# Optimization experiments

Measured on AMD Instinct MI355X. Metric: run time of the kernel, lower is better.

## Reference

```python
import jax, jax.numpy as jnp
import numpy as np

# canonical SMPL kinematic tree (24 joints)
PARENTS = [-1, 0, 0, 0, 1, 2, 3, 4, 5, 6, 7, 8, 9, 9, 9, 12, 13, 14, 16, 17, 18, 19, 20, 21]
B, V, J, NB = 512, 6890, 24, 10


def setup_inputs() -> dict:
    key = jax.random.key(0)
    ks = jax.random.split(key, 9)
    betas = jax.random.normal(ks[0], (B, NB), jnp.float32)
    body_pose = 0.3 * jax.random.normal(ks[1], (B, (J - 1) * 3), jnp.float32)
    global_orient = 0.3 * jax.random.normal(ks[2], (B, 3), jnp.float32)
    transl = jax.random.normal(ks[3], (B, 3), jnp.float32)
    v_template = jax.random.normal(ks[4], (V, 3), jnp.float32)
    shapedirs = 0.01 * jax.random.normal(ks[5], (V, 3, NB), jnp.float32)
    posedirs = 0.01 * jax.random.normal(ks[6], (9 * (J - 1), V * 3), jnp.float32)
    J_regressor = jax.nn.softmax(4.0 * jax.random.normal(ks[7], (J, V), jnp.float32), axis=-1)
    lbs_weights = jax.nn.softmax(4.0 * jax.random.normal(ks[8], (V, J), jnp.float32), axis=-1)
    return {"betas": betas, "body_pose": body_pose, "global_orient": global_orient,
            "transl": transl, "v_template": v_template, "shapedirs": shapedirs,
            "posedirs": posedirs, "J_regressor": J_regressor, "lbs_weights": lbs_weights}


def rodrigues(rot_vecs):
    # rot_vecs: [B, J, 3] axis-angle -> [B, J, 3, 3] rotation matrices
    angle = jnp.linalg.norm(rot_vecs + 1e-8, axis=-1, keepdims=True)  # [B,J,1]
    axis = rot_vecs / angle
    s = jnp.sin(angle)[..., None]
    c = jnp.cos(angle)[..., None]
    x, y, z = axis[..., 0], axis[..., 1], axis[..., 2]
    zeros = jnp.zeros_like(x)
    K = jnp.stack([zeros, -z, y, z, zeros, -x, -y, x, zeros], axis=-1)
    K = K.reshape(rot_vecs.shape[:-1] + (3, 3))
    ident = jnp.eye(3, dtype=rot_vecs.dtype)
    return ident + s * K + (1.0 - c) * (K @ K)


def lbs(betas, full_pose, v_template, shapedirs, posedirs, J_regressor, lbs_weights):
    b = betas.shape[0]
    dtype = betas.dtype
    # shape blendshapes: [B,V,3]
    v_shaped = v_template[None] + jnp.einsum('bl,vkl->bvk', betas, shapedirs)
    # rest joints: [B,J,3]
    Jrest = jnp.einsum('jv,bvk->bjk', J_regressor, v_shaped)
    # pose -> rotation matrices [B,J,3,3]
    rot_mats = rodrigues(full_pose.reshape(b, -1, 3))
    ident = jnp.eye(3, dtype=dtype)
    pose_feature = (rot_mats[:, 1:] - ident).reshape(b, -1)  # [B,207]
    v_posed = v_shaped + (pose_feature @ posedirs).reshape(b, V, 3)
    # relative joint locations along the tree
    parents = np.asarray(PARENTS)
    rel_J = Jrest.at[:, 1:].add(-Jrest[:, parents[1:]])
    # local 4x4 transforms [B,J,4,4]
    T34 = jnp.concatenate([rot_mats, rel_J[..., None]], axis=-1)  # [B,J,3,4]
    bottom = jnp.broadcast_to(jnp.array([0, 0, 0, 1], dtype=dtype), (b, J, 1, 4))
    T_local = jnp.concatenate([T34, bottom], axis=-2)
    # sequential chain over the fixed 24-joint kinematic tree
    chain = [T_local[:, 0]]
    for i in range(1, J):
        chain.append(chain[parents[i]] @ T_local[:, i])
    Tg = jnp.stack(chain, axis=1)  # [B,J,4,4]
    posed_joints = Tg[:, :, :3, 3]
    # remove rest-pose joint contribution: A = Tg - pack(Tg[:, :, :3, :3] @ Jrest)
    corr = jnp.einsum('bjmn,bjn->bjm', Tg[:, :, :3, :3], Jrest)  # [B,J,3]
    corr4 = jnp.concatenate([corr, jnp.zeros((b, J, 1), dtype=dtype)], axis=-1)
    A = Tg.at[..., 3].add(-corr4)
    # skinning: per-vertex transform [B,V,4,4]
    T = jnp.einsum('vj,bjmn->bvmn', lbs_weights, A)
    v_h = jnp.concatenate([v_posed, jnp.ones((b, V, 1), dtype=dtype)], axis=-1)
    verts = jnp.einsum('bvmn,bvn->bvm', T, v_h)[..., :3]
    return verts, posed_joints


def reference(betas, body_pose, global_orient, transl, v_template, shapedirs,
              posedirs, J_regressor, lbs_weights):
    full_pose = jnp.concatenate([global_orient, body_pose], axis=1)  # [B,72]
    vertices, joints = lbs(betas, full_pose, v_template, shapedirs, posedirs,
                           J_regressor, lbs_weights)
    vertices = vertices + transl[:, None, :]
    joints = joints + transl[:, None, :]
    return vertices, joints
```

## Files before the change

kernel.cpp:

```cpp
#include <hip/hip_runtime.h>
#include <math.h>

#define B_    512
#define V_    6890
#define J_    24
#define NB_   10
#define K_    207
#define KPAD  224
#define NCOL  20670
#define TV    32
#define TC    96
#define CPAD  20736
#define NCVT  2268
#define SPD_STRIDE 232
#define VP_STRIDE  100

typedef __attribute__((ext_vector_type(8))) __bf16 bf16x8;
typedef __attribute__((ext_vector_type(4))) float  f32x4;

__constant__ int c_par[24] = {-1,0,0,0,1,2,3,4,5,6,7,8,9,9,9,12,13,14,16,17,18,19,20,21};
__constant__ int c_lev[24] = { 0,1,1,1,2,2,2,3,3,3,4,4,4,4,4, 5, 5, 5, 6, 6, 7, 7, 8, 8};

__device__ __forceinline__ unsigned short f2bf(float x) {
    union { float f; unsigned u; } v; v.f = x;
    unsigned r = (v.u + 0x7FFFu + ((v.u >> 16) & 1u)) >> 16;
    return (unsigned short)r;
}
__device__ __forceinline__ float bf2f(unsigned short h) {
    union { unsigned u; float f; } v; v.u = (unsigned)h << 16;
    return v.f;
}
__device__ __forceinline__ void wsync() {
    asm volatile("s_waitcnt lgkmcnt(0)" ::: "memory");
}

__global__ __launch_bounds__(256) void k_pre(const float* __restrict__ pd,
                                             const float* __restrict__ sd,
                                             const float* __restrict__ Jreg,
                                             const float* __restrict__ vt,
                                             unsigned short* __restrict__ pdT,
                                             float* __restrict__ JS,
                                             float* __restrict__ JT,
                                             int do_cvt)
{
    const int tid = threadIdx.x;
    const int bx  = blockIdx.x;

    if (bx < NCVT) {
        if (!do_cvt) return;
        const int c  = (bx % 324) * 64 + (tid & 63);
        const int kq = (bx / 324) * 4 + (tid >> 6);
        unsigned short u[8];
#pragma unroll
        for (int e = 0; e < 8; ++e) {
            const int k = kq * 8 + e;
            float x = 0.f;
            if (c < NCOL) {
                if (k < K_)            x = pd[(size_t)k * NCOL + c];
                else if (k < K_ + NB_) x = sd[(size_t)c * NB_ + (k - K_)];
            }
            u[e] = f2bf(x);
        }
        *reinterpret_cast<uint4*>(&pdT[(size_t)c * KPAD + kq * 8]) =
            *reinterpret_cast<const uint4*>(u);
        return;
    }

    const int jk = bx - NCVT;
    const int j = jk / 3, k = jk % 3;
    float acc[11];
#pragma unroll
    for (int i = 0; i < 11; ++i) acc[i] = 0.f;

#pragma unroll 4
    for (int v = tid; v < V_; v += 256) {
        const float r = Jreg[j * V_ + v];
        acc[0] = fmaf(r, vt[v * 3 + k], acc[0]);
        const float* s = &sd[(v * 3 + k) * NB_];
#pragma unroll
        for (int l = 0; l < NB_; ++l) acc[1 + l] = fmaf(r, s[l], acc[1 + l]);
    }

    __shared__ float red[4][11];
    const int lane = tid & 63, w = tid >> 6;
#pragma unroll
    for (int i = 0; i < 11; ++i) {
        float a = acc[i];
        for (int off = 32; off; off >>= 1) a += __shfl_xor(a, off, 64);
        acc[i] = a;
    }
    if (lane == 0) {
#pragma unroll
        for (int i = 0; i < 11; ++i) red[w][i] = acc[i];
    }
    __syncthreads();
    if (tid == 0) {
        for (int i = 0; i < 11; ++i) {
            const float s = red[0][i] + red[1][i] + red[2][i] + red[3][i];
            if (i == 0) JT[j * 3 + k] = s;
            else        JS[(j * 3 + k) * NB_ + (i - 1)] = s;
        }
    }
}

__global__ __launch_bounds__(256) void k_pose(const float* __restrict__ betas,
                                              const float* __restrict__ body_pose,
                                              const float* __restrict__ global_orient,
                                              const float* __restrict__ transl,
                                              const float* __restrict__ JS,
                                              const float* __restrict__ JT,
                                              unsigned short* __restrict__ Atout,
                                              unsigned short* __restrict__ pfout,
                                              float* __restrict__ joints_out)
{
    const int wv   = threadIdx.x >> 6;
    const int j    = threadIdx.x & 63;
    const int b    = blockIdx.x * 4 + wv;

    __shared__ float sR[4][24][9];
    __shared__ float sJ[4][24][3];
    __shared__ float sTl[4][24][12];
    __shared__ float sTg[4][24][12];

    if (j < 24) {
        float rx, ry, rz;
        if (j == 0) {
            rx = global_orient[b * 3 + 0];
            ry = global_orient[b * 3 + 1];
            rz = global_orient[b * 3 + 2];
        } else {
            const float* p = &body_pose[b * 69 + (j - 1) * 3];
            rx = p[0]; ry = p[1]; rz = p[2];
        }
        const float ax = rx + 1e-8f, ay = ry + 1e-8f, az = rz + 1e-8f;
        const float angle = sqrtf(ax * ax + ay * ay + az * az);
        const float inv = 1.f / angle;
        const float x = rx * inv, y = ry * inv, z = rz * inv;
        const float s = sinf(angle), c = cosf(angle), t = 1.f - c;

        float R[9];
        R[0] = 1.f - t * (y * y + z * z);
        R[1] = -s * z + t * x * y;
        R[2] =  s * y + t * x * z;
        R[3] =  s * z + t * x * y;
        R[4] = 1.f - t * (x * x + z * z);
        R[5] = -s * x + t * y * z;
        R[6] = -s * y + t * x * z;
        R[7] =  s * x + t * y * z;
        R[8] = 1.f - t * (x * x + y * y);

#pragma unroll
        for (int e = 0; e < 9; ++e) sR[wv][j][e] = R[e];

        if (j >= 1) {
#pragma unroll
            for (int e = 0; e < 9; ++e) {
                const float id = (e == 0 || e == 4 || e == 8) ? 1.f : 0.f;
                pfout[b * KPAD + (j - 1) * 9 + e] = f2bf(R[e] - id);
            }
        }
#pragma unroll
        for (int k = 0; k < 3; ++k) {
            float jr = JT[j * 3 + k];
#pragma unroll
            for (int l = 0; l < NB_; ++l)
                jr = fmaf(betas[b * NB_ + l], JS[(j * 3 + k) * NB_ + l], jr);
            sJ[wv][j][k] = jr;
        }
    }
    if (j < KPAD - K_) {
        const float val = (j < NB_) ? betas[b * NB_ + j] : 0.f;
        pfout[b * KPAD + K_ + j] = f2bf(val);
    }
    wsync();

    if (j < 24) {
        const int p = c_par[j];
        float t0 = sJ[wv][j][0], t1 = sJ[wv][j][1], t2 = sJ[wv][j][2];
        if (j > 0) { t0 -= sJ[wv][p][0]; t1 -= sJ[wv][p][1]; t2 -= sJ[wv][p][2]; }
        sTl[wv][j][0] = sR[wv][j][0]; sTl[wv][j][1] = sR[wv][j][1];
        sTl[wv][j][2] = sR[wv][j][2]; sTl[wv][j][3] = t0;
        sTl[wv][j][4] = sR[wv][j][3]; sTl[wv][j][5] = sR[wv][j][4];
        sTl[wv][j][6] = sR[wv][j][5]; sTl[wv][j][7] = t1;
        sTl[wv][j][8] = sR[wv][j][6]; sTl[wv][j][9] = sR[wv][j][7];
        sTl[wv][j][10] = sR[wv][j][8]; sTl[wv][j][11] = t2;
    }
    wsync();

    if (j == 0) {
#pragma unroll
        for (int e = 0; e < 12; ++e) sTg[wv][0][e] = sTl[wv][0][e];
    }
    wsync();

    for (int lev = 1; lev <= 8; ++lev) {
        if (j < 24 && c_lev[j] == lev) {
            const int p = c_par[j];
            float o[12];
#pragma unroll
            for (int r = 0; r < 3; ++r) {
#pragma unroll
                for (int c = 0; c < 4; ++c) {
                    float v = (c == 3) ? sTg[wv][p][r * 4 + 3] : 0.f;
#pragma unroll
                    for (int m = 0; m < 3; ++m)
                        v = fmaf(sTg[wv][p][r * 4 + m], sTl[wv][j][m * 4 + c], v);
                    o[r * 4 + c] = v;
                }
            }
#pragma unroll
            for (int e = 0; e < 12; ++e) sTg[wv][j][e] = o[e];
        }
        wsync();
    }

    if (j < 24) {
        float corr[3];
#pragma unroll
        for (int r = 0; r < 3; ++r)
            corr[r] = sTg[wv][j][r * 4 + 0] * sJ[wv][j][0]
                    + sTg[wv][j][r * 4 + 1] * sJ[wv][j][1]
                    + sTg[wv][j][r * 4 + 2] * sJ[wv][j][2];

#pragma unroll
        for (int r = 0; r < 3; ++r) {
            float row[4];
            row[0] = sTg[wv][j][r * 4 + 0];
            row[1] = sTg[wv][j][r * 4 + 1];
            row[2] = sTg[wv][j][r * 4 + 2];
            row[3] = sTg[wv][j][r * 4 + 3] - corr[r] + transl[b * 3 + r];
#pragma unroll
            for (int cc = 0; cc < 4; ++cc) {
                const float val = row[cc];
                const unsigned short hi = f2bf(val);
                const unsigned short lo = f2bf(val - bf2f(hi));
                const size_t base = ((size_t)b * 16 + r * 4 + cc) * 64;
                Atout[base + j]      = hi;
                Atout[base + 32 + j] = lo;
            }
        }
#pragma unroll
        for (int k = 0; k < 3; ++k)
            joints_out[(b * 24 + j) * 3 + k] = sTg[wv][j][k * 4 + 3] + transl[b * 3 + k];
    }
    for (int idx = j; idx < 1024; idx += 64) {
        const int e = idx >> 6, jj = idx & 63;
        if (e >= 12 || (jj & 31) >= 24)
            Atout[((size_t)b * 16 + e) * 64 + jj] = 0;
    }
}

template<bool PRE>
__global__ __launch_bounds__(256, 3) void k_verts(
    const float* __restrict__ v_template,
    const float* __restrict__ posedirs,
    const float* __restrict__ shapedirs,
    const unsigned short* __restrict__ pdT,
    const float* __restrict__ lbs_weights,
    const unsigned short* __restrict__ pf,
    const unsigned short* __restrict__ At,
    float* __restrict__ out)
{
    __shared__ __align__(16) char smem[44544 + 2048];
    unsigned short* s_pd = (unsigned short*)smem;
    unsigned short* s_w  = (unsigned short*)(smem + 44544);
    float*          s_vp = (float*)smem;

    const int tid = threadIdx.x;
    const int l   = tid & 63;
    const int wv  = tid >> 6;
    const int m   = l & 15;
    const int g   = l >> 4;

    const int lraw  = blockIdx.x;
    const int gl    = (lraw & 7) * 216 + (lraw >> 3);
    const int vtile = gl >> 3;
    const int btile = gl & 7;
    const int vbase = vtile * TV;
    const int bbase = btile * 64;
    const int vb3   = vtile * TC;

    if (tid < 128) {
        const int v  = tid >> 2, jq = tid & 3;
        const int vv = vbase + v;
        const int vc = vv < V_ ? vv : V_ - 1;
        unsigned short u[8];
        if (jq < 3) {
            const float* src = &lbs_weights[vc * 24 + jq * 8];
#pragma unroll
            for (int e = 0; e < 8; ++e) u[e] = f2bf(src[e]);
        } else {
#pragma unroll
            for (int e = 0; e < 8; ++e) u[e] = 0;
        }
        *reinterpret_cast<uint4*>(&s_w[v * 32 + jq * 8]) =
            *reinterpret_cast<const uint4*>(u);
    }

#pragma unroll
    for (int i = 0; i < 11; ++i) {
        const int idx = i * 256 + tid;
        if (i == 10 && tid >= 128) break;
        const int col = idx / 28, kq = idx % 28;
        uint4 val;
        if (PRE) {
            val = *reinterpret_cast<const uint4*>(
                &pdT[(size_t)(vb3 + col) * KPAD + kq * 8]);
        } else {
            unsigned short u[8];
            const int c = vb3 + col;
#pragma unroll
            for (int e = 0; e < 8; ++e) {
                const int k = kq * 8 + e;
                float x = 0.f;
                if (c < NCOL) {
                    if (k < K_)            x = posedirs[(size_t)k * NCOL + c];
                    else if (k < K_ + NB_) x = shapedirs[(size_t)c * NB_ + (k - K_)];
                }
                u[e] = f2bf(x);
            }
            val = *reinterpret_cast<const uint4*>(u);
        }
        *reinterpret_cast<uint4*>(&s_pd[col * SPD_STRIDE + kq * 8]) = val;
    }

    bf16x8 af[7];
#pragma unroll
    for (int ck = 0; ck < 7; ++ck)
        af[ck] = *reinterpret_cast<const bf16x8*>(
            &pf[(size_t)(bbase + wv * 16 + m) * KPAD + ck * 32 + g * 8]);

    __syncthreads();

    f32x4 acc1[6];
#pragma unroll
    for (int i = 0; i < 6; ++i) acc1[i] = (f32x4){0.f, 0.f, 0.f, 0.f};

#pragma unroll
    for (int ck = 0; ck < 7; ++ck) {
        const unsigned short* pb = &s_pd[m * SPD_STRIDE + ck * 32 + g * 8];
#pragma unroll
        for (int nt = 0; nt < 6; ++nt) {
            const bf16x8 bfr = *reinterpret_cast<const bf16x8*>(
                &pb[nt * 16 * SPD_STRIDE]);
            acc1[nt] = __builtin_amdgcn_mfma_f32_16x16x32_bf16(af[ck], bfr, acc1[nt], 0, 0, 0);
        }
    }

    __syncthreads();

    float* vp = &s_vp[wv * 16 * VP_STRIDE];
#pragma unroll
    for (int nt = 0; nt < 6; ++nt) {
        const int c = vb3 + nt * 16 + m;
        const float vtf = (c < NCOL) ? v_template[c] : 0.f;
#pragma unroll
        for (int r = 0; r < 4; ++r)
            vp[(g * 4 + r) * VP_STRIDE + nt * 16 + m] = acc1[nt][r] + vtf;
    }
    wsync();

    bf16x8 wf[2];
#pragma unroll
    for (int nt = 0; nt < 2; ++nt)
        wf[nt] = *reinterpret_cast<const bf16x8*>(&s_w[(nt * 16 + m) * 32 + g * 8]);

    const int b0 = bbase + wv * 16;
    bf16x8 phi[2], plo[2];
#pragma unroll
    for (int p = 0; p < 2; ++p) {
        const size_t arow = ((size_t)(b0 + p) * 16 + m) * 64;
        phi[p] = *reinterpret_cast<const bf16x8*>(&At[arow + g * 8]);
        plo[p] = *reinterpret_cast<const bf16x8*>(&At[arow + 32 + g * 8]);
    }

#pragma unroll
    for (int mt8 = 0; mt8 < 16; ++mt8) {
        const bf16x8 ahi = phi[mt8 & 1], alo = plo[mt8 & 1];
        if (mt8 < 14) {
            const size_t arow = ((size_t)(b0 + mt8 + 2) * 16 + m) * 64;
            phi[mt8 & 1] = *reinterpret_cast<const bf16x8*>(&At[arow + g * 8]);
            plo[mt8 & 1] = *reinterpret_cast<const bf16x8*>(&At[arow + 32 + g * 8]);
        }
        const int b = b0 + mt8;
#pragma unroll
        for (int nt = 0; nt < 2; ++nt) {
            f32x4 t = (f32x4){0.f, 0.f, 0.f, 0.f};
            t = __builtin_amdgcn_mfma_f32_16x16x32_bf16(ahi, wf[nt], t, 0, 0, 0);
            t = __builtin_amdgcn_mfma_f32_16x16x32_bf16(alo, wf[nt], t, 0, 0, 0);
            const float vpx = vp[mt8 * VP_STRIDE + nt * 48 + 3 * m + 0];
            const float vpy = vp[mt8 * VP_STRIDE + nt * 48 + 3 * m + 1];
            const float vpz = vp[mt8 * VP_STRIDE + nt * 48 + 3 * m + 2];
            const float o = fmaf(t[0], vpx, fmaf(t[1], vpy, fmaf(t[2], vpz, t[3])));
            const int vv = vbase + nt * 16 + m;
            if (g < 3 && vv < V_)
                out[((size_t)b * V_ + vv) * 3 + g] = o;
        }
    }
}

extern "C" void kernel_launch(void* const* d_in, const int* in_sizes, int n_in,
                              void* d_out, int out_size, void* d_ws, size_t ws_size,
                              hipStream_t stream)
{
    const float* betas         = (const float*)d_in[0];
    const float* body_pose     = (const float*)d_in[1];
    const float* global_orient = (const float*)d_in[2];
    const float* transl        = (const float*)d_in[3];
    const float* v_template    = (const float*)d_in[4];
    const float* shapedirs     = (const float*)d_in[5];
    const float* posedirs      = (const float*)d_in[6];
    const float* J_regressor   = (const float*)d_in[7];
    const float* lbs_weights   = (const float*)d_in[8];

    float* out = (float*)d_out;
    float* ws  = (float*)d_ws;

    float* JS = ws;
    float* JT = ws + 720;
    unsigned short* pfw = (unsigned short*)(ws + 792);
    unsigned short* Atw = pfw + (size_t)B_ * KPAD;
    unsigned short* pdT = Atw + (size_t)B_ * 16 * 64;

    const size_t needed_pre = 792u * 4 + (size_t)B_ * KPAD * 2
                            + (size_t)B_ * 16 * 64 * 2
                            + (size_t)CPAD * KPAD * 2;
    const bool pre = (ws_size >= needed_pre);

    float* joints = out + (size_t)B_ * V_ * 3;

    k_pre <<<NCVT + 72, 256, 0, stream>>>(posedirs, shapedirs, J_regressor,
                                          v_template, pdT, JS, JT, pre ? 1 : 0);
    k_pose<<<B_ / 4, 256, 0, stream>>>(betas, body_pose, global_orient, transl,
                                       JS, JT, Atw, pfw, joints);
    if (pre) {
        k_verts<true><<<1728, 256, 0, stream>>>(v_template, posedirs, shapedirs,
                                                pdT, lbs_weights, pfw, Atw, out);
    } else {
        k_verts<false><<<1728, 256, 0, stream>>>(v_template, posedirs, shapedirs,
                                                 pdT, lbs_weights, pfw, Atw, out);
    }
}
```

Measured before the change: 76.98 us.

## Split fused vertex kernel into blend GEMM and skinning kernels via workspace

Splits the fused vertex kernel into two kernels. k_g1 computes the pose and shape blend GEMM and writes v_posed (512x20736 floats) to a workspace buffer. k_lbs reads it back and applies the skinning with a different tile shape (64 vertices x 32 batches) and higher occupancy. The aim is to decouple the two stages' tiling and occupancy needs, at the cost of an extra round trip through global memory of roughly 42MB and an extra launch. The fallback path keeps the fused kernel, and the workspace requirement grows.

Measured after the change: 85.46 us. 1.11x slower.

```diff
diff --git a/kernel.cpp b/kernel.cpp
--- a/kernel.cpp
+++ b/kernel.cpp
@@ -13,7 +13,7 @@
 #define CPAD  20736
 #define NCVT  2268
 #define SPD_STRIDE 232
-#define VP_STRIDE  100
+#define VP_STRIDE  104
 
 typedef __attribute__((ext_vector_type(8))) __bf16 bf16x8;
 typedef __attribute__((ext_vector_type(4))) float  f32x4;
@@ -250,12 +250,169 @@
     }
 }
 
-template<bool PRE>
-__global__ __launch_bounds__(256, 3) void k_verts(
+__global__ __launch_bounds__(256, 3) void k_g1(
+    const float* __restrict__ v_template,
+    const unsigned short* __restrict__ pdT,
+    const unsigned short* __restrict__ pf,
+    float* __restrict__ vp_ws)
+{
+    __shared__ __align__(16) char smem[44544];
+    unsigned short* s_pd = (unsigned short*)smem;
+    float*          s_vp = (float*)smem;
+
+    const int tid = threadIdx.x;
+    const int l   = tid & 63;
+    const int wv  = tid >> 6;
+    const int m   = l & 15;
+    const int g   = l >> 4;
+
+    const int lraw  = blockIdx.x;
+    const int gl    = (lraw & 7) * 216 + (lraw >> 3);
+    const int vtile = gl >> 3;
+    const int btile = gl & 7;
+    const int bbase = btile * 64;
+    const int vb3   = vtile * TC;
+
+#pragma unroll
+    for (int i = 0; i < 11; ++i) {
+        const int idx = i * 256 + tid;
+        if (i == 10 && tid >= 128) break;
+        const int col = idx / 28, kq = idx % 28;
+        const uint4 val = *reinterpret_cast<const uint4*>(
+            &pdT[(size_t)(vb3 + col) * KPAD + kq * 8]);
+        *reinterpret_cast<uint4*>(&s_pd[col * SPD_STRIDE + kq * 8]) = val;
+    }
+
+    bf16x8 af[7];
+#pragma unroll
+    for (int ck = 0; ck < 7; ++ck)
+        af[ck] = *reinterpret_cast<const bf16x8*>(
+            &pf[(size_t)(bbase + wv * 16 + m) * KPAD + ck * 32 + g * 8]);
+
+    __syncthreads();
+
+    f32x4 acc1[6];
+#pragma unroll
+    for (int i = 0; i < 6; ++i) acc1[i] = (f32x4){0.f, 0.f, 0.f, 0.f};
+
+#pragma unroll
+    for (int ck = 0; ck < 7; ++ck) {
+        const unsigned short* pb = &s_pd[m * SPD_STRIDE + ck * 32 + g * 8];
+#pragma unroll
+        for (int nt = 0; nt < 6; ++nt) {
+            const bf16x8 bfr = *reinterpret_cast<const bf16x8*>(
+                &pb[nt * 16 * SPD_STRIDE]);
+            acc1[nt] = __builtin_amdgcn_mfma_f32_16x16x32_bf16(af[ck], bfr, acc1[nt], 0, 0, 0);
+        }
+    }
+
+    __syncthreads();
+
+    float* vp = &s_vp[wv * 16 * VP_STRIDE];
+#pragma unroll
+    for (int nt = 0; nt < 6; ++nt) {
+        const int c = vb3 + nt * 16 + m;
+        const float vtf = (c < NCOL) ? v_template[c] : 0.f;
+#pragma unroll
+        for (int r = 0; r < 4; ++r)
+            vp[(g * 4 + r) * VP_STRIDE + nt * 16 + m] = acc1[nt][r] + vtf;
+    }
+    wsync();
+
+    const int b0 = bbase + wv * 16;
+#pragma unroll
+    for (int i = 0; i < 6; ++i) {
+        const int idx = i * 64 + l;
+        const int rb = idx / 24, q = idx % 24;
+        const uint4 val = *reinterpret_cast<const uint4*>(&vp[rb * VP_STRIDE + q * 4]);
+        *reinterpret_cast<uint4*>(&vp_ws[(size_t)(b0 + rb) * CPAD + vb3 + q * 4]) = val;
+    }
+}
+
+__global__ __launch_bounds__(256, 6) void k_lbs(
+    const float* __restrict__ lbs_weights,
+    const unsigned short* __restrict__ At,
+    const float* __restrict__ vp_ws,
+    float* __restrict__ out)
+{
+    __shared__ unsigned short s_w[64 * 32];
+
+    const int tid = threadIdx.x;
+    const int l   = tid & 63;
+    const int wv  = tid >> 6;
+    const int m   = l & 15;
+    const int g   = l >> 4;
+
+    const int lraw  = blockIdx.x;
+    const int gl    = (lraw & 7) * 216 + (lraw >> 3);
+    const int vtile = gl >> 4;
+    const int btile = gl & 15;
+    const int vbase = vtile * 64;
+    const int bbase = btile * 32;
+    const int vb3   = vtile * 192;
+
+    {
+        const int v  = tid >> 2, jq = tid & 3;
+        const int vv = vbase + v;
+        const int vc = vv < V_ ? vv : V_ - 1;
+        unsigned short u[8];
+        if (jq < 3) {
+            const float* src = &lbs_weights[vc * 24 + jq * 8];
+#pragma unroll
+            for (int e = 0; e < 8; ++e) u[e] = f2bf(src[e]);
+        } else {
+#pragma unroll
+            for (int e = 0; e < 8; ++e) u[e] = 0;
+        }
+        *reinterpret_cast<uint4*>(&s_w[v * 32 + jq * 8]) =
+            *reinterpret_cast<const uint4*>(u);
+    }
+    __syncthreads();
+
+    bf16x8 wf[4];
+#pragma unroll
+    for (int nt = 0; nt < 4; ++nt)
+        wf[nt] = *reinterpret_cast<const bf16x8*>(&s_w[(nt * 16 + m) * 32 + g * 8]);
+
+    const int b0 = bbase + wv * 8;
+    bf16x8 phi[2], plo[2];
+#pragma unroll
+    for (int p = 0; p < 2; ++p) {
+        const size_t arow = ((size_t)(b0 + p) * 16 + m) * 64;
+        phi[p] = *reinterpret_cast<const bf16x8*>(&At[arow + g * 8]);
+        plo[p] = *reinterpret_cast<const bf16x8*>(&At[arow + 32 + g * 8]);
+    }
+
+#pragma unroll
+    for (int mt = 0; mt < 8; ++mt) {
+        const bf16x8 ahi = phi[mt & 1], alo = plo[mt & 1];
+        if (mt < 6) {
+            const size_t arow = ((size_t)(b0 + mt + 2) * 16 + m) * 64;
+            phi[mt & 1] = *reinterpret_cast<const bf16x8*>(&At[arow + g * 8]);
+            plo[mt & 1] = *reinterpret_cast<const bf16x8*>(&At[arow + 32 + g * 8]);
+        }
+        const int b = b0 + mt;
+        const float* __restrict__ vpb = &vp_ws[(size_t)b * CPAD + vb3];
+#pragma unroll
+        for (int nt = 0; nt < 4; ++nt) {
+            f32x4 t = (f32x4){0.f, 0.f, 0.f, 0.f};
+            t = __builtin_amdgcn_mfma_f32_16x16x32_bf16(ahi, wf[nt], t, 0, 0, 0);
+            t = __builtin_amdgcn_mfma_f32_16x16x32_bf16(alo, wf[nt], t, 0, 0, 0);
+            const float vpx = vpb[nt * 48 + 3 * m + 0];
+            const float vpy = vpb[nt * 48 + 3 * m + 1];
+            const float vpz = vpb[nt * 48 + 3 * m + 2];
+            const float o = fmaf(t[0], vpx, fmaf(t[1], vpy, fmaf(t[2], vpz, t[3])));
+            const int vv = vbase + nt * 16 + m;
+            if (g < 3 && vv < V_)
+                out[((size_t)b * V_ + vv) * 3 + g] = o;
+        }
+    }
+}
+
+__global__ __launch_bounds__(256, 3) void k_fused_fb(
     const float* __restrict__ v_template,
     const float* __restrict__ posedirs,
     const float* __restrict__ shapedirs,
-    const unsigned short* __restrict__ pdT,
     const float* __restrict__ lbs_weights,
     const unsigned short* __restrict__ pf,
     const unsigned short* __restrict__ At,
@@ -302,26 +459,20 @@
         const int idx = i * 256 + tid;
         if (i == 10 && tid >= 128) break;
         const int col = idx / 28, kq = idx % 28;
-        uint4 val;
-        if (PRE) {
-            val = *reinterpret_cast<const uint4*>(
-                &pdT[(size_t)(vb3 + col) * KPAD + kq * 8]);
-        } else {
-            unsigned short u[8];
-            const int c = vb3 + col;
-#pragma unroll
-            for (int e = 0; e < 8; ++e) {
-                const int k = kq * 8 + e;
-                float x = 0.f;
-                if (c < NCOL) {
-                    if (k < K_)            x = posedirs[(size_t)k * NCOL + c];
-                    else if (k < K_ + NB_) x = shapedirs[(size_t)c * NB_ + (k - K_)];
-                }
-                u[e] = f2bf(x);
+        unsigned short u[8];
+        const int c = vb3 + col;
+#pragma unroll
+        for (int e = 0; e < 8; ++e) {
+            const int k = kq * 8 + e;
+            float x = 0.f;
+            if (c < NCOL) {
+                if (k < K_)            x = posedirs[(size_t)k * NCOL + c];
+                else if (k < K_ + NB_) x = shapedirs[(size_t)c * NB_ + (k - K_)];
             }
-            val = *reinterpret_cast<const uint4*>(u);
-        }
-        *reinterpret_cast<uint4*>(&s_pd[col * SPD_STRIDE + kq * 8]) = val;
+            u[e] = f2bf(x);
+        }
+        *reinterpret_cast<uint4*>(&s_pd[col * SPD_STRIDE + kq * 8]) =
+            *reinterpret_cast<const uint4*>(u);
     }
 
     bf16x8 af[7];
@@ -335,18 +486,15 @@
     f32x4 acc1[6];
 #pragma unroll
     for (int i = 0; i < 6; ++i) acc1[i] = (f32x4){0.f, 0.f, 0.f, 0.f};
-
 #pragma unroll
     for (int ck = 0; ck < 7; ++ck) {
         const unsigned short* pb = &s_pd[m * SPD_STRIDE + ck * 32 + g * 8];
 #pragma unroll
         for (int nt = 0; nt < 6; ++nt) {
-            const bf16x8 bfr = *reinterpret_cast<const bf16x8*>(
-                &pb[nt * 16 * SPD_STRIDE]);
+            const bf16x8 bfr = *reinterpret_cast<const bf16x8*>(&pb[nt * 16 * SPD_STRIDE]);
             acc1[nt] = __builtin_amdgcn_mfma_f32_16x16x32_bf16(af[ck], bfr, acc1[nt], 0, 0, 0);
         }
     }
-
     __syncthreads();
 
     float* vp = &s_vp[wv * 16 * VP_STRIDE];
@@ -373,7 +521,6 @@
         phi[p] = *reinterpret_cast<const bf16x8*>(&At[arow + g * 8]);
         plo[p] = *reinterpret_cast<const bf16x8*>(&At[arow + 32 + g * 8]);
     }
-
 #pragma unroll
     for (int mt8 = 0; mt8 < 16; ++mt8) {
         const bf16x8 ahi = phi[mt8 & 1], alo = plo[mt8 & 1];
@@ -421,11 +568,13 @@
     unsigned short* pfw = (unsigned short*)(ws + 792);
     unsigned short* Atw = pfw + (size_t)B_ * KPAD;
     unsigned short* pdT = Atw + (size_t)B_ * 16 * 64;
-
-    const size_t needed_pre = 792u * 4 + (size_t)B_ * KPAD * 2
-                            + (size_t)B_ * 16 * 64 * 2
-                            + (size_t)CPAD * KPAD * 2;
-    const bool pre = (ws_size >= needed_pre);
+    float* vpw = (float*)(pdT + (size_t)CPAD * KPAD);
+
+    const size_t needed = 792u * 4 + (size_t)B_ * KPAD * 2
+                        + (size_t)B_ * 16 * 64 * 2
+                        + (size_t)CPAD * KPAD * 2
+                        + (size_t)B_ * CPAD * 4;
+    const bool pre = (ws_size >= needed);
 
     float* joints = out + (size_t)B_ * V_ * 3;
 
@@ -434,10 +583,10 @@
     k_pose<<<B_ / 4, 256, 0, stream>>>(betas, body_pose, global_orient, transl,
                                        JS, JT, Atw, pfw, joints);
     if (pre) {
-        k_verts<true><<<1728, 256, 0, stream>>>(v_template, posedirs, shapedirs,
-                                                pdT, lbs_weights, pfw, Atw, out);
+        k_g1 <<<1728, 256, 0, stream>>>(v_template, pdT, pfw, vpw);
+        k_lbs<<<1728, 256, 0, stream>>>(lbs_weights, Atw, vpw, out);
     } else {
-        k_verts<false><<<1728, 256, 0, stream>>>(v_template, posedirs, shapedirs,
-                                                 pdT, lbs_weights, pfw, Atw, out);
-    }
-}
+        k_fused_fb<<<1728, 256, 0, stream>>>(v_template, posedirs, shapedirs,
+                                             lbs_weights, pfw, Atw, out);
+    }
+}
```
